# Optimization experiments

Measured on AMD Instinct MI355X. Metric: run time of the kernel, lower is better.

## Reference

```python
import jax, jax.numpy as jnp
import numpy as np

TOPK_FRAC = 0.05  # init arg `topk` (fraction of pool kept)


def setup_inputs() -> dict:
    key = jax.random.key(0)
    k1, k2 = jax.random.split(key)
    x = jax.random.normal(k1, (16, 256, 32, 32), dtype=jnp.float32)
    # nn.Parameter(torch.rand(P, C)) -> uniform [0, 1)
    visual_concept_pool = jax.random.uniform(k2, (2048, 256), dtype=jnp.float32)
    return {"x": x, "visual_concept_pool": visual_concept_pool}


def reference(x, visual_concept_pool):
    n, c, h, w = x.shape
    P = visual_concept_pool.shape[0]
    L = h * w
    xf = x.reshape(n, c, L)                              # [n, c, L]
    # dot_product[n, P, L] = pool @ xf
    dot = jnp.einsum('pc,ncl->npl', visual_concept_pool, xf)
    pool_norm = jnp.sqrt(jnp.sum(visual_concept_pool ** 2, axis=1))   # [P]
    x_norm = jnp.sqrt(jnp.sum(xf ** 2, axis=1))                        # [n, L]
    cos = dot / (pool_norm[None, :, None] * x_norm[:, None, :])       # [n, P, L]

    # mode 1.1: top-k over the pool dimension per (n, pixel)
    keep = int(TOPK_FRAC * P)
    cos_t = jnp.transpose(cos, (0, 2, 1))                # [n, L, P]
    _, idx = jax.lax.top_k(jnp.abs(cos_t), keep)         # [n, L, keep]
    mask = jnp.zeros_like(cos_t).at[
        jnp.arange(n)[:, None, None],
        jnp.arange(L)[None, :, None],
        idx,
    ].set(1.0)                                           # [n, L, P]
    masked = cos_t * mask
    normed = masked / jnp.sum(masked, axis=-1, keepdims=True)  # renormalize over P
    # reconstruct[n, c, L] = pool^T @ cos
    recon = jnp.einsum('pc,nlp->ncl', visual_concept_pool, normed)
    return recon.reshape(n, c, h, w)
```

## Files before the change

kernel.cpp:

```cpp
#include <hip/hip_runtime.h>
#include <hip/hip_fp16.h>

typedef unsigned short u16;
typedef _Float16 half8 __attribute__((ext_vector_type(8)));
typedef float floatx4 __attribute__((ext_vector_type(4)));

#define C_DIM 256
#define P_DIM 2048
#define L_DIM 1024
#define N_DIM 16
#define KEEP 102
#define KPAD 104
#define QTR_PIX 4096
#define SCALE 256.0f

__device__ __forceinline__ void st8(u16* dst, const u16* s) {
  uint4 u;
  u.x = (unsigned)s[0] | ((unsigned)s[1] << 16);
  u.y = (unsigned)s[2] | ((unsigned)s[3] << 16);
  u.z = (unsigned)s[4] | ((unsigned)s[5] << 16);
  u.w = (unsigned)s[6] | ((unsigned)s[7] << 16);
  *(uint4*)dst = u;
}

__device__ __forceinline__ u16 f2h_ftz(float v) {
  if (fabsf(v) < 6.103515625e-5f) return 0;
  return __half_as_ushort(__float2half(v));
}

__device__ __forceinline__ void gl_lds16(const u16* g, u16* l) {
  __builtin_amdgcn_global_load_lds(
      (const __attribute__((address_space(1))) unsigned int*)g,
      (__attribute__((address_space(3))) unsigned int*)l, 16, 0, 0);
}

union SMem {
  u16 sB[2][2][8][512];
  struct {
    float tbuf[8][260];
    int2  kpw[8][KPAD];
  } sel;
};

__device__ __forceinline__ void packpool_body(int b,
                                              const float* __restrict__ pool,
                                              u16* __restrict__ ah,
                                              u16* __restrict__ al,
                                              u16* __restrict__ ph) {
  __shared__ float ppart[8][16];
  int tid = b * 512 + threadIdx.x;
  int lane = tid & 63;
  int ks = (tid >> 6) & 7;
  int w = threadIdx.x >> 6;
  int pm = tid >> 9;
  int p = pm * 16 + (lane & 15);
  int c0 = ks * 32 + ((lane >> 4) << 3);
  const float* src = pool + (size_t)p * C_DIM + c0;

  float raw[8];
  float part = 0.f;
#pragma unroll
  for (int j = 0; j < 8; ++j) {
    raw[j] = src[j];
    part += raw[j] * raw[j];
  }
  part += __shfl_xor(part, 16);
  part += __shfl_xor(part, 32);
  if (lane < 16) ppart[w][lane] = part;
  __syncthreads();
  float s = 0.f;
#pragma unroll
  for (int w2 = 0; w2 < 8; ++w2) s += ppart[w2][lane & 15];
  float sc = (1.0f / sqrtf(s)) * SCALE;

  u16 h8[8], l8[8], p8[8];
#pragma unroll
  for (int j = 0; j < 8; ++j) {
    float rawj = raw[j];
    p8[j] = __half_as_ushort(__float2half(rawj));
    float v = rawj * sc;
    u16 h = f2h_ftz(v);
    float r = v - __half2float(__ushort_as_half(h));
    h8[j] = h;
    l8[j] = f2h_ftz(r);
  }
  size_t o = (size_t)tid * 8;
  st8(ah + o, h8); st8(al + o, l8);
  st8(ph + (size_t)p * C_DIM + c0, p8);
}

__device__ __forceinline__ void packx_body(int pb, int pq,
                                           const float* __restrict__ x,
                                           u16* __restrict__ xh,
                                           u16* __restrict__ xl) {
  int t = threadIdx.x;
  int lane = t & 63;
  int ks = (t >> 6) & 7;
  int pn = pq * 256 + pb;
  int pix = pn * 16 + (lane & 15);
  int n = pix >> 10, l = pix & 1023;
  int c0 = ks * 32 + ((lane >> 4) << 3);
  const float* src = x + ((size_t)(n * C_DIM + c0)) * L_DIM + l;
  u16 h8[8], l8[8];
#pragma unroll
  for (int j = 0; j < 8; ++j) {
    float v = src[(size_t)j * L_DIM] * SCALE;
    u16 h = f2h_ftz(v);
    float r = v - __half2float(__ushort_as_half(h));
    h8[j] = h;
    l8[j] = f2h_ftz(r);
  }
  size_t o = ((size_t)pn * 512 + (size_t)ks * 64 + lane) * 8;
  st8(xh + o, h8); st8(xl + o, l8);
}

__global__ __launch_bounds__(512) void k_pre(const float* __restrict__ pool,
                                             u16* __restrict__ ah,
                                             u16* __restrict__ al,
                                             u16* __restrict__ ph,
                                             const float* __restrict__ x,
                                             u16* __restrict__ xh,
                                             u16* __restrict__ xl) {
  int b = blockIdx.x;
  if (b < 128) packpool_body(b, pool, ah, al, ph);
  else packx_body(b - 128, 0, x, xh, xl);
}

__device__ __forceinline__ void mfma_body(int b, int mq,
                                          const u16* __restrict__ ah_,
                                          const u16* __restrict__ al_,
                                          const u16* __restrict__ xh_,
                                          const u16* __restrict__ xl_,
                                          float* __restrict__ sbuf,
                                          u16 (*sB)[2][8][512]) {
  const int t = threadIdx.x, lane = t & 63, w = t >> 6;
  const int pT = b & 15, pixT = b >> 4;
  const int pm = pT * 8 + w;
  const int pnBase = mq * 256 + pixT * 8;
  const half8* A8h = (const half8*)ah_;
  const half8* A8l = (const half8*)al_;
  const u16* xsrc[2] = {xh_, xl_};

  floatx4 acc[8];
#pragma unroll
  for (int nt = 0; nt < 8; ++nt) acc[nt] = (floatx4){0.f, 0.f, 0.f, 0.f};

#pragma unroll
  for (int q = 0; q < 2; ++q) {
    int id = w * 2 + q;
    int arr = id >> 3, nt = id & 7;
    gl_lds16(xsrc[arr] + ((size_t)(pnBase + nt) * 512 + lane) * 8,
             &sB[0][arr][nt][0]);
  }
  __syncthreads();

#pragma unroll 1
  for (int ks = 0; ks < 8; ++ks) {
    const int cur = ks & 1;
    half8 aH, aL;
    {
      size_t idx = (size_t)pm * 512 + (size_t)ks * 64 + lane;
      aH = A8h[idx]; aL = A8l[idx];
    }
    if (ks < 7) {
#pragma unroll
      for (int q = 0; q < 2; ++q) {
        int id = w * 2 + q;
        int arr = id >> 3, nt = id & 7;
        gl_lds16(xsrc[arr] + ((size_t)(pnBase + nt) * 512 + (ks + 1) * 64 + lane) * 8,
                 &sB[cur ^ 1][arr][nt][0]);
      }
    }
#pragma unroll
    for (int nt = 0; nt < 8; ++nt) {
      half8 bh = *(const half8*)&sB[cur][0][nt][lane * 8];
      half8 bl = *(const half8*)&sB[cur][1][nt][lane * 8];
      floatx4 c = acc[nt];
      c = __builtin_amdgcn_mfma_f32_16x16x32_f16(aH, bh, c, 0, 0, 0);
      c = __builtin_amdgcn_mfma_f32_16x16x32_f16(aH, bl, c, 0, 0, 0);
      c = __builtin_amdgcn_mfma_f32_16x16x32_f16(aL, bh, c, 0, 0, 0);
      acc[nt] = c;
    }
    __syncthreads();
  }

  const int qr = lane >> 4, cl = lane & 15;
  const int pix0 = pixT * 128;
  const int pcol = pT * 128 + w * 16;
#pragma unroll
  for (int nt = 0; nt < 8; ++nt) {
    float* dst = sbuf + (size_t)(pix0 + nt * 16 + cl) * P_DIM + pcol + qr * 4;
    *(float4*)dst = make_float4(acc[nt][0], acc[nt][1], acc[nt][2], acc[nt][3]);
  }
}

__device__ __forceinline__ void select_body(int b, int sq,
                                            const float* __restrict__ sbuf,
                                            const u16* __restrict__ pool_h,
                                            float* __restrict__ out,
                                            float (*tbuf)[260],
                                            int2 (*kpw)[KPAD]) {
  const int t = threadIdx.x;
  const int lane = t & 63;
  const int wv = t >> 6;
  const int gp0 = sq * QTR_PIX + b * 8;
  const int n = gp0 >> 10;
  const int l0 = gp0 & 1023;
  const float* sp = sbuf + (size_t)(b * 8 + wv) * P_DIM;

  float4 v[8];
#pragma unroll
  for (int q = 0; q < 8; ++q) v[q] = *(const float4*)(sp + q * 256 + lane * 4);

  if (lane < KPAD - KEEP) kpw[wv][KEEP + lane] = make_int2(0, 0);

  float M = 0.f;
#pragma unroll
  for (int q = 0; q < 8; ++q) {
    M = fmaxf(M, fabsf(v[q].x)); M = fmaxf(M, fabsf(v[q].y));
    M = fmaxf(M, fabsf(v[q].z)); M = fmaxf(M, fabsf(v[q].w));
  }
#pragma unroll
  for (int off = 1; off < 64; off <<= 1) M = fmaxf(M, __shfl_xor(M, off));
  const unsigned bitsM = __float_as_uint(M);

  auto countGE = [&](float mf) -> unsigned {
    unsigned cnt = 0;
#pragma unroll
    for (int q = 0; q < 8; ++q) {
      cnt += (unsigned)__popcll(__ballot(fabsf(v[q].x) >= mf));
      cnt += (unsigned)__popcll(__ballot(fabsf(v[q].y) >= mf));
      cnt += (unsigned)__popcll(__ballot(fabsf(v[q].z) >= mf));
      cnt += (unsigned)__popcll(__ballot(fabsf(v[q].w) >= mf));
    }
    return cnt;
  };

  const unsigned t1 = (bitsM > (1u << 23)) ? bitsM - (1u << 23) : 1u;
  const unsigned t2 = (bitsM > (2u << 23)) ? bitsM - (2u << 23) : 1u;
  const unsigned t3 = (bitsM > (3u << 23)) ? bitsM - (3u << 23) : 1u;
  const unsigned t4 = (bitsM > (5u << 23)) ? bitsM - (5u << 23) : 1u;
  const float g1 = __uint_as_float(t1), g2 = __uint_as_float(t2);
  const float g3 = __uint_as_float(t3), g4 = __uint_as_float(t4);
  unsigned c1 = 0, c2 = 0, c3 = 0, c4 = 0;
#pragma unroll
  for (int q = 0; q < 8; ++q) {
    const float* f = (const float*)&v[q];
#pragma unroll
    for (int rr = 0; rr < 4; ++rr) {
      float av = fabsf(f[rr]);
      c1 += (unsigned)__popcll(__ballot(av >= g1));
      c2 += (unsigned)__popcll(__ballot(av >= g2));
      c3 += (unsigned)__popcll(__ballot(av >= g3));
      c4 += (unsigned)__popcll(__ballot(av >= g4));
    }
  }

  unsigned lo = 0u, hi = 1u, cl_ = P_DIM, ch_ = 0u;
  bool exact = false;
  if (c1 == (unsigned)KEEP)      { lo = t1; exact = true; }
  else if (c2 == (unsigned)KEEP) { lo = t2; exact = true; }
  else if (c3 == (unsigned)KEEP) { lo = t3; exact = true; }
  else if (c4 == (unsigned)KEEP) { lo = t4; exact = true; }
  else if (c1 > (unsigned)KEEP)  { lo = t1; cl_ = c1; hi = bitsM + 1u; ch_ = 0u; }
  else if (c2 > (unsigned)KEEP)  { lo = t2; cl_ = c2; hi = t1; ch_ = c1; }
  else if (c3 > (unsigned)KEEP)  { lo = t3; cl_ = c3; hi = t2; ch_ = c2; }
  else if (c4 > (unsigned)KEEP)  { lo = t4; cl_ = c4; hi = t3; ch_ = c3; }
  else                           { lo = 0u; cl_ = P_DIM; hi = t4; ch_ = c4; }

  int it = 0;
  while (!exact && hi - lo > 1u) {
    unsigned span = hi - lo;
    unsigned step;
    if ((it++ & 1) == 0) {
      step = (unsigned)((float)span * (float)(cl_ - KEEP) / (float)(cl_ - ch_));
    } else {
      step = span >> 1;
    }
    if (step < 1u) step = 1u;
    else if (step > span - 1u) step = span - 1u;
    unsigned m = lo + step;
    unsigned cnt = countGE(__uint_as_float(m));
    if (cnt == (unsigned)KEEP) { lo = m; exact = true; break; }
    if (cnt > (unsigned)KEEP) { lo = m; cl_ = cnt; } else { hi = m; ch_ = cnt; }
  }
  const float V = __uint_as_float(lo);
  const float Vp = exact ? V : __uint_as_float(lo + 1u);

  unsigned rrem = 0u;
  if (!exact) {
    unsigned gt = countGE(Vp);
    rrem = (unsigned)KEEP - gt;
  }

  unsigned gmask[8], tmask[8];
#pragma unroll
  for (int q = 0; q < 8; ++q) {
    const float* f = (const float*)&v[q];
    unsigned gm = 0, tm = 0;
#pragma unroll
    for (int rr = 0; rr < 4; ++rr) {
      float av = fabsf(f[rr]);
      if (av >= Vp) gm |= (1u << rr);
      else if (av >= V) tm |= (1u << rr);
    }
    gmask[q] = gm; tmask[q] = tm;
  }

  const unsigned long long lowm = (1ull << lane) - 1ull;
  unsigned base = 0, tiebase = 0;
  float Ssum = 0.f;
#pragma unroll
  for (int q = 0; q < 8; ++q) {
    const float* f = (const float*)&v[q];
    unsigned km = gmask[q];
    if (rrem != 0u) {
      unsigned teq = 0, myeqb = 0;
#pragma unroll
      for (int rr = 0; rr < 4; ++rr) {
        unsigned long long beq = __ballot((tmask[q] >> rr) & 1u);
        teq += (unsigned)__popcll(beq);
        myeqb += (unsigned)__popcll(beq & lowm);
      }
      unsigned cum = 0;
#pragma unroll
      for (int rr = 0; rr < 4; ++rr) {
        if ((tmask[q] >> rr) & 1u) {
          if (tiebase + myeqb + cum < rrem) km |= (1u << rr);
          ++cum;
        }
      }
      tiebase += teq;
    }
    unsigned long long bk[4];
    unsigned tot = 0, myb = 0;
#pragma unroll
    for (int rr = 0; rr < 4; ++rr) {
      bk[rr] = __ballot((km >> rr) & 1u);
      tot += (unsigned)__popcll(bk[rr]);
      myb += (unsigned)__popcll(bk[rr] & lowm);
    }
    {
      unsigned cum = 0;
#pragma unroll
      for (int rr = 0; rr < 4; ++rr) {
        if ((km >> rr) & 1u) {
          unsigned pos = base + myb + cum;
          kpw[wv][pos] = make_int2((q * 256 + lane * 4 + rr) << 9,
                                   __float_as_int(f[rr]));
          Ssum += f[rr];
          ++cum;
        }
      }
    }
    base += tot;
  }

#pragma unroll
  for (int off = 1; off < 64; off <<= 1) Ssum += __shfl_xor(Ssum, off);
  const float invS = 1.0f / Ssum;

  __builtin_amdgcn_wave_barrier();

  float a0 = 0.f, a1 = 0.f, a2 = 0.f, a3 = 0.f;
  const char* pb = (const char*)(pool_h + 4 * lane);
  int2 eA[4], eB[4];
  uint2 rA[4], rB[4];

  auto PROC = [&](const int2* e, const uint2* r) {
#pragma unroll
    for (int j = 0; j < 4; ++j) {
      float w2 = __int_as_float(e[j].y);
      unsigned rx = r[j].x, ry = r[j].y;
      asm volatile("v_fma_mix_f32 %0, %1, %2, %0 op_sel:[0,0,0] op_sel_hi:[0,1,0]"
                   : "+v"(a0) : "v"(w2), "v"(rx));
      asm volatile("v_fma_mix_f32 %0, %1, %2, %0 op_sel:[0,1,0] op_sel_hi:[0,1,0]"
                   : "+v"(a1) : "v"(w2), "v"(rx));
      asm volatile("v_fma_mix_f32 %0, %1, %2, %0 op_sel:[0,0,0] op_sel_hi:[0,1,0]"
                   : "+v"(a2) : "v"(w2), "v"(ry));
      asm volatile("v_fma_mix_f32 %0, %1, %2, %0 op_sel:[0,1,0] op_sel_hi:[0,1,0]"
                   : "+v"(a3) : "v"(w2), "v"(ry));
    }
  };

#pragma unroll
  for (int j = 0; j < 4; ++j) eA[j] = kpw[wv][j];
#pragma unroll
  for (int j = 0; j < 4; ++j) rA[j] = *(const uint2*)(pb + (unsigned)eA[j].x);
#pragma unroll 1
  for (int k = 0; k < KPAD; k += 8) {
    const int kb = k + 4;
#pragma unroll
    for (int j = 0; j < 4; ++j) eB[j] = kpw[wv][kb + j];
#pragma unroll
    for (int j = 0; j < 4; ++j) rB[j] = *(const uint2*)(pb + (unsigned)eB[j].x);
    PROC(eA, rA);
    const int ka = (k + 8 < KPAD) ? k + 8 : 0;
#pragma unroll
    for (int j = 0; j < 4; ++j) eA[j] = kpw[wv][ka + j];
#pragma unroll
    for (int j = 0; j < 4; ++j) rA[j] = *(const uint2*)(pb + (unsigned)eA[j].x);
    PROC(eB, rB);
  }
  a0 *= invS; a1 *= invS; a2 *= invS; a3 *= invS;

  *(float4*)&tbuf[wv][4 * lane] = make_float4(a0, a1, a2, a3);
  __syncthreads();

  {
    int c = t >> 1, lq = t & 1;
    float4 o = make_float4(tbuf[4 * lq + 0][c], tbuf[4 * lq + 1][c],
                           tbuf[4 * lq + 2][c], tbuf[4 * lq + 3][c]);
    *(float4*)(out + ((size_t)(n * C_DIM + c)) * L_DIM + l0 + 4 * lq) = o;
  }
}

__global__ __launch_bounds__(512, 4) void k_main(const u16* __restrict__ ah_,
                                                 const u16* __restrict__ al_,
                                                 const u16* __restrict__ xh_,
                                                 const u16* __restrict__ xl_,
                                                 const u16* __restrict__ ph,
                                                 const float* __restrict__ x,
                                                 float* __restrict__ sbuf0,
                                                 float* __restrict__ sbuf1,
                                                 float* __restrict__ out,
                                                 int mq, int sq, int pq) {
  __shared__ __align__(16) SMem sm;
  const int b = blockIdx.x;
  const int nsel = (sq >= 0) ? 512 : 0;
  const int npk = (pq >= 0) ? 256 : 0;
  if (b < nsel) {
    select_body(b, sq, (sq & 1) ? sbuf1 : sbuf0, ph, out,
                sm.sel.tbuf, sm.sel.kpw);
  } else if (b < nsel + npk) {
    packx_body(b - nsel, pq, x, (u16*)xh_, (u16*)xl_);
  } else {
    mfma_body(b - nsel - npk, mq, ah_, al_, xh_, xl_, (mq & 1) ? sbuf1 : sbuf0, sm.sB);
  }
}

extern "C" void kernel_launch(void* const* d_in, const int* in_sizes, int n_in,
                              void* d_out, int out_size, void* d_ws, size_t ws_size,
                              hipStream_t stream) {
  const float* x = (const float*)d_in[0];
  const float* pool = (const float*)d_in[1];
  float* out = (float*)d_out;
  char* wsb = (char*)d_ws;
  float* sbuf0 = (float*)wsb;
  float* sbuf1 = (float*)(wsb + 33554432);
  u16* xh = (u16*)(wsb + 67108864);
  u16* xl = xh + 4194304;
  u16* ah = xl + 4194304;
  u16* al = ah + 524288;
  u16* ph = al + 524288;

  k_pre<<<384, 512, 0, stream>>>(pool, ah, al, ph, x, xh, xl);

  k_main<<<768, 512, 0, stream>>>(ah, al, xh, xl, ph, x, sbuf0, sbuf1, out, 0, -1, 1);
  k_main<<<1280, 512, 0, stream>>>(ah, al, xh, xl, ph, x, sbuf0, sbuf1, out, 1, 0, 2);
  k_main<<<1280, 512, 0, stream>>>(ah, al, xh, xl, ph, x, sbuf0, sbuf1, out, 2, 1, 3);
  k_main<<<1024, 512, 0, stream>>>(ah, al, xh, xl, ph, x, sbuf0, sbuf1, out, 3, 2, -1);
  k_main<<<512, 512, 0, stream>>>(ah, al, xh, xl, ph, x, sbuf0, sbuf1, out, -1, 3, -1);
}
```

Measured before the change: 243.5 us.

## Rebalance pipelined stage chunks with non-uniform sizes across launches

Replaces the fixed quarter-sized pipeline stages with parameterized per-launch ranges for the GEMM, select and pack work. The first stage is smaller and later stages are larger, and the scratch buffers grow to hold the bigger chunks. The aim is to shorten the pipeline fill and drain and keep the grid load more even across the five launches. The uneven chunk bookkeeping has to stay consistent, or pixels will be skipped or written twice.

```diff
diff --git a/kernel.cpp b/kernel.cpp
--- a/kernel.cpp
+++ b/kernel.cpp
@@ -11,7 +11,6 @@
 #define N_DIM 16
 #define KEEP 102
 #define KPAD 104
-#define QTR_PIX 4096
 #define SCALE 256.0f
 
 __device__ __forceinline__ void st8(u16* dst, const u16* s) {
@@ -89,14 +88,14 @@
   st8(ph + (size_t)p * C_DIM + c0, p8);
 }
 
-__device__ __forceinline__ void packx_body(int pb, int pq,
+__device__ __forceinline__ void packx_body(int pb, int pn0,
                                            const float* __restrict__ x,
                                            u16* __restrict__ xh,
                                            u16* __restrict__ xl) {
   int t = threadIdx.x;
   int lane = t & 63;
   int ks = (t >> 6) & 7;
-  int pn = pq * 256 + pb;
+  int pn = pn0 + pb;
   int pix = pn * 16 + (lane & 15);
   int n = pix >> 10, l = pix & 1023;
   int c0 = ks * 32 + ((lane >> 4) << 3);
@@ -126,7 +125,7 @@
   else packx_body(b - 128, 0, x, xh, xl);
 }
 
-__device__ __forceinline__ void mfma_body(int b, int mq,
+__device__ __forceinline__ void mfma_body(int b, int pn0,
                                           const u16* __restrict__ ah_,
                                           const u16* __restrict__ al_,
                                           const u16* __restrict__ xh_,
@@ -136,7 +135,7 @@
   const int t = threadIdx.x, lane = t & 63, w = t >> 6;
   const int pT = b & 15, pixT = b >> 4;
   const int pm = pT * 8 + w;
-  const int pnBase = mq * 256 + pixT * 8;
+  const int pnBase = pn0 + pixT * 8;
   const half8* A8h = (const half8*)ah_;
   const half8* A8l = (const half8*)al_;
   const u16* xsrc[2] = {xh_, xl_};
@@ -194,7 +193,7 @@
   }
 }
 
-__device__ __forceinline__ void select_body(int b, int sq,
+__device__ __forceinline__ void select_body(int b, int gp0base,
                                             const float* __restrict__ sbuf,
                                             const u16* __restrict__ pool_h,
                                             float* __restrict__ out,
@@ -203,7 +202,7 @@
   const int t = threadIdx.x;
   const int lane = t & 63;
   const int wv = t >> 6;
-  const int gp0 = sq * QTR_PIX + b * 8;
+  const int gp0 = gp0base + b * 8;
   const int n = gp0 >> 10;
   const int l0 = gp0 & 1023;
   const float* sp = sbuf + (size_t)(b * 8 + wv) * P_DIM;
@@ -421,21 +420,20 @@
                                                  const u16* __restrict__ xl_,
                                                  const u16* __restrict__ ph,
                                                  const float* __restrict__ x,
-                                                 float* __restrict__ sbuf0,
-                                                 float* __restrict__ sbuf1,
+                                                 float* __restrict__ msbuf,
+                                                 const float* __restrict__ ssbuf,
                                                  float* __restrict__ out,
-                                                 int mq, int sq, int pq) {
+                                                 int m_pn0, int m_nblk,
+                                                 int s_gp0, int s_nblk,
+                                                 int p_pn0, int p_nblk) {
   __shared__ __align__(16) SMem sm;
   const int b = blockIdx.x;
-  const int nsel = (sq >= 0) ? 512 : 0;
-  const int npk = (pq >= 0) ? 256 : 0;
-  if (b < nsel) {
-    select_body(b, sq, (sq & 1) ? sbuf1 : sbuf0, ph, out,
-                sm.sel.tbuf, sm.sel.kpw);
-  } else if (b < nsel + npk) {
-    packx_body(b - nsel, pq, x, (u16*)xh_, (u16*)xl_);
+  if (b < s_nblk) {
+    select_body(b, s_gp0, ssbuf, ph, out, sm.sel.tbuf, sm.sel.kpw);
+  } else if (b < s_nblk + p_nblk) {
+    packx_body(b - s_nblk, p_pn0, x, (u16*)xh_, (u16*)xl_);
   } else {
-    mfma_body(b - nsel - npk, mq, ah_, al_, xh_, xl_, (mq & 1) ? sbuf1 : sbuf0, sm.sB);
+    mfma_body(b - s_nblk - p_nblk, m_pn0, ah_, al_, xh_, xl_, msbuf, sm.sB);
   }
 }
 
@@ -446,19 +444,24 @@
   const float* pool = (const float*)d_in[1];
   float* out = (float*)d_out;
   char* wsb = (char*)d_ws;
-  float* sbuf0 = (float*)wsb;
-  float* sbuf1 = (float*)(wsb + 33554432);
-  u16* xh = (u16*)(wsb + 67108864);
+  float* sb0 = (float*)wsb;
+  float* sb1 = (float*)(wsb + 37748736);
+  u16* xh = (u16*)(wsb + 75497472);
   u16* xl = xh + 4194304;
   u16* ah = xl + 4194304;
   u16* al = ah + 524288;
   u16* ph = al + 524288;
 
-  k_pre<<<384, 512, 0, stream>>>(pool, ah, al, ph, x, xh, xl);
-
-  k_main<<<768, 512, 0, stream>>>(ah, al, xh, xl, ph, x, sbuf0, sbuf1, out, 0, -1, 1);
-  k_main<<<1280, 512, 0, stream>>>(ah, al, xh, xl, ph, x, sbuf0, sbuf1, out, 1, 0, 2);
-  k_main<<<1280, 512, 0, stream>>>(ah, al, xh, xl, ph, x, sbuf0, sbuf1, out, 2, 1, 3);
-  k_main<<<1024, 512, 0, stream>>>(ah, al, xh, xl, ph, x, sbuf0, sbuf1, out, 3, 2, -1);
-  k_main<<<512, 512, 0, stream>>>(ah, al, xh, xl, ph, x, sbuf0, sbuf1, out, -1, 3, -1);
-}
+  k_pre<<<288, 512, 0, stream>>>(pool, ah, al, ph, x, xh, xl);
+
+  k_main<<<608, 512, 0, stream>>>(ah, al, xh, xl, ph, x, sb0, sb0, out,
+                                  0, 320, 0, 0, 160, 288);
+  k_main<<<1184, 512, 0, stream>>>(ah, al, xh, xl, ph, x, sb1, sb0, out,
+                                   160, 576, 0, 320, 448, 288);
+  k_main<<<1440, 512, 0, stream>>>(ah, al, xh, xl, ph, x, sb0, sb1, out,
+                                   448, 576, 2560, 576, 736, 288);
+  k_main<<<1152, 512, 0, stream>>>(ah, al, xh, xl, ph, x, sb1, sb0, out,
+                                   736, 576, 7168, 576, 0, 0);
+  k_main<<<576, 512, 0, stream>>>(ah, al, xh, xl, ph, x, sb0, sb1, out,
+                                  0, 0, 11776, 576, 0, 0);
+}
```

Measured after the change: 238.6 us. -2.0%, faster.
